# Kernel optimization log

Measured on AMD Instinct MI355X. Metric: run time of the kernel, lower is better.

## Reference

```python
import jax, jax.numpy as jnp
import numpy as np
import math

B, NH, DIM = 8, 12, 768
NP, NF = 196, 16            # n (patches per frame), num_frames
DH = DIM // NH              # 64
D3 = 3 * DH                 # per-head feature dim after projection (192)
SEQ = NP * NF               # 3136 body tokens (+1 cls)
ROT = DH                    # rotary dim (RotaryEmbedding(dim=64))
SCALE = 1.0 / (math.sqrt(DH) * NH)


def _heads(t):
    b, s, _ = t.shape
    return t.reshape(b, s, NH, D3).transpose(0, 2, 1, 3)  # b h s d


def _rope(x):
    # lucidrains-style interleaved rotary on the first ROT dims of each head
    s = x.shape[2]
    inv_freq = 1.0 / (10000.0 ** (jnp.arange(0, ROT, 2, dtype=jnp.float32) / ROT))
    freqs = jnp.arange(s, dtype=jnp.float32)[:, None] * inv_freq  # [s, ROT/2]
    freqs = jnp.repeat(freqs, 2, axis=-1)                          # [s, ROT]
    cos, sin = jnp.cos(freqs), jnp.sin(freqs)
    xr, xp = x[..., :ROT], x[..., ROT:]
    x1, x2 = xr[..., ::2], xr[..., 1::2]
    half = jnp.stack((-x2, x1), axis=-1).reshape(xr.shape)
    return jnp.concatenate([xr * cos + half * sin, xp], axis=-1)


def _att_sum(q, k, v):
    # softmax(q k^T * SCALE) v, then sum over queries keepdim (dim 2)
    p = jax.nn.softmax(jnp.einsum('bhqd,bhkd->bhqk', q, k) * SCALE, axis=-1)
    return jnp.einsum('bhqk,bhkd->bhqd', p, v).sum(axis=2, keepdims=True)


def setup_inputs():
    key = jax.random.key(0)
    ks = jax.random.split(key, 11)
    p = lambda k, sh: jax.random.normal(k, sh, jnp.float32) * 0.02
    return {
        'x': jax.random.normal(ks[0], (B, SEQ + 1, DIM), jnp.float32),
        'Wq': p(ks[1], (DIM, 3 * DIM)), 'bq': p(ks[2], (3 * DIM,)),
        'Wk': p(ks[3], (DIM, 3 * DIM)), 'bk': p(ks[4], (3 * DIM,)),
        'Wv': p(ks[5], (DIM, 3 * DIM)), 'bv': p(ks[6], (3 * DIM,)),
        'Wt': p(ks[7], (3 * DIM, DIM)), 'bt': p(ks[8], (DIM,)),
        'Wf': p(ks[9], (3 * DIM, DIM)), 'bf': p(ks[10], (DIM,)),
    }


def reference(x, Wq, bq, Wk, bk, Wv, bv, Wt, bt, Wf, bf):
    body = x[:, 1:, :]
    # NOTE: the original swaps k/v projections for body tokens (k_mat uses self.v, v_mat uses self.k)
    q = _rope(_heads(body @ Wq + bq))
    k = _rope(_heads(body @ Wv + bv))
    v = _heads(body @ Wk + bk)

    # cls-token attention over the full sequence (correct k/v mapping here)
    q_cls = _heads(x[:, 0:1, :] @ Wq + bq)          # [b,h,1,d]
    k_cls = _heads(x @ Wk + bk)
    v_cls = _heads(x @ Wv + bv)
    p_cls = jax.nn.softmax(jnp.einsum('bhqd,bhkd->bhqk', q_cls, k_cls) * SCALE, axis=-1)
    cls_out = jnp.einsum('bhqk,bhkd->bhqd', p_cls, v_cls)  # [b,h,1,d]

    # temporal attention per spatial position x = 1..NP-1, vectorized
    # token index t = f*NP + x  ->  reshape [b,h,NF,NP,d], move spatial first
    qg = q.reshape(B, NH, NF, NP, D3).transpose(0, 1, 3, 2, 4)[:, :, 1:]  # [b,h,NP-1,NF,d]
    kg = k.reshape(B, NH, NF, NP, D3).transpose(0, 1, 3, 2, 4)[:, :, 1:]
    vg = v.reshape(B, NH, NF, NP, D3).transpose(0, 1, 3, 2, 4)[:, :, 1:]
    pg = jax.nn.softmax(jnp.einsum('bhxfd,bhxgd->bhxfg', qg, kg) * SCALE, axis=-1)
    tmp = jnp.einsum('bhxfg,bhxgd->bhxfd', pg, vg).sum(axis=3)  # sum over query frames -> [b,h,NP-1,d]

    temporal = jnp.tile(tmp, (1, 1, NF, 1))  # torch .repeat tiles -> [b,h,(NP-1)*NF,d]
    ti = temporal.transpose(0, 2, 1, 3).reshape(B, (NP - 1) * NF, NH * D3) @ Wt + bt

    # second pass (q uses self.q, v uses self.k, k uses self.v per original)
    q2 = _heads(ti @ Wq + bq)
    v2 = _heads(ti @ Wk + bk)
    k2 = _heads(ti @ Wv + bv)
    outs = [_att_sum(q2[:, :, 0:NP], k2[:, :, 0:NP], v2[:, :, 0:NP])]
    for xi in range(1, NF):  # small fixed loop over frames
        outs.append(_att_sum(q2[:, :, xi:xi + NP], k2[:, :, xi::NP], v2[:, :, xi::NP]))
    t2 = jnp.concatenate(outs, axis=2)        # [b,h,NF,d]
    t2 = jnp.tile(t2, (1, 1, NP, 1))          # [b,h,SEQ,d]
    t2 = jnp.concatenate([cls_out, t2], axis=2)  # [b,h,SEQ+1,d]
    return t2.transpose(0, 2, 1, 3).reshape(B, SEQ + 1, NH * D3) @ Wf + bf
```

## Files before the change

kernel.cpp:

```cpp
#include <hip/hip_runtime.h>
#include <cstdint>
#include <cstddef>


typedef unsigned short u16;
typedef __attribute__((ext_vector_type(8))) short short8;
typedef __attribute__((ext_vector_type(4))) float f32x4;

#define DEV static __device__ __forceinline__
#define AS1 __attribute__((address_space(1)))
#define AS3 __attribute__((address_space(3)))

DEV float b2f(u16 u) { union { unsigned int i; float f; } v; v.i = ((unsigned int)u) << 16; return v.f; }
DEV float b2fs(short s) { return b2f((u16)s); }
DEV u16 f2b(float f) {
    union { float f; unsigned int i; } v; v.f = f;
    unsigned int r = v.i + 0x7fffu + ((v.i >> 16) & 1u);
    return (u16)(r >> 16);
}
DEV void gld16(const u16* g, u16* l) {
    __builtin_amdgcn_global_load_lds((AS1 void*)(g), (AS3 void*)(l), 16, 0, 0);
}

DEV int detect_fl(const u16* x) {
    int lane = threadIdx.x & 63;
    const u16* p = x + lane * 8;
    int c = 0;
#pragma unroll
    for (int j = 0; j < 8; j++) c += (((p[j] >> 7) & 0xFFu) >= 134u);
#pragma unroll
    for (int off = 32; off; off >>= 1) c += __shfl_xor(c, off);
    return c > 8;
}

constexpr int   ROWS  = 3137;
constexpr int   NPm1  = 195;
constexpr int   MT    = 8 * NPm1;
constexpr int   N3    = 2304;
constexpr float SCALE = 1.0f / 96.0f;
constexpr size_t P2Z  = (size_t)MT * N3;
constexpr int   CLS_NS = 32;
constexpr int   CLS_RS = 99;
constexpr int   LDK   = 200;

DEV float wave_max(float v) {
#pragma unroll
    for (int off = 32; off; off >>= 1) v = fmaxf(v, __shfl_xor(v, off));
    return v;
}
DEV float wave_sum(float v) {
#pragma unroll
    for (int off = 32; off; off >>= 1) v += __shfl_xor(v, off);
    return v;
}
DEV float block_max256(float v, float* red) {
    v = wave_max(v);
    __syncthreads();
    if ((threadIdx.x & 63) == 0) red[threadIdx.x >> 6] = v;
    __syncthreads();
    return fmaxf(fmaxf(red[0], red[1]), fmaxf(red[2], red[3]));
}
DEV float block_sum256(float v, float* red) {
    v = wave_sum(v);
    __syncthreads();
    if ((threadIdx.x & 63) == 0) red[threadIdx.x >> 6] = v;
    __syncthreads();
    return (red[0] + red[1]) + (red[2] + red[3]);
}

DEV void do_transpose(const void* in, u16* out, int R, int C,
                      int bx, int by, int fl, u16 (*tls)[33]) {
    int tx = threadIdx.x & 31, ty = threadIdx.x >> 5;
#pragma unroll
    for (int i = 0; i < 32; i += 8) {
        int r = by + ty + i, c = bx + tx;
        size_t idx = (size_t)r * C + c;
        tls[ty + i][tx] = fl ? f2b(((const float*)in)[idx]) : ((const u16*)in)[idx];
    }
    __syncthreads();
#pragma unroll
    for (int i = 0; i < 32; i += 8) {
        int c = bx + ty + i, r = by + tx;
        out[(size_t)c * R + r] = tls[tx][ty + i];
    }
}

__global__ __launch_bounds__(256) void prep(const u16* __restrict__ x,
                                            const void* __restrict__ Wq,
                                            const void* __restrict__ Wk,
                                            const void* __restrict__ Wv,
                                            const void* __restrict__ Wt,
                                            const void* __restrict__ Wf,
                                            u16* __restrict__ WT,
                                            u16* __restrict__ WtT,
                                            u16* __restrict__ WfT,
                                            u16* __restrict__ xb,
                                            float* __restrict__ wacc,
                                            float* __restrict__ ropeT,
                                            int usexb) {
    __shared__ u16 tls[32][33];
    int bid = blockIdx.x;
    if (bid < 5184) {
        int fl = detect_fl(x);
        int z = bid / 1728, t = bid % 1728;
        const void* W = (z == 0) ? Wq : (z == 1) ? Wk : Wv;
        do_transpose(W, WT + (size_t)z * N3 * 768, 768, N3,
                     (t % 72) * 32, (t / 72) * 32, fl, tls);
        return;
    }
    bid -= 5184;
    if (bid < 3456) {
        int fl = detect_fl(x);
        int z = bid / 1728, t = bid % 1728;
        do_transpose(z ? Wf : Wt, z ? WfT : WtT, N3, 768,
                     (t % 24) * 32, (t / 24) * 32, fl, tls);
        return;
    }
    bid -= 3456;
    if (bid < 9411) {
        if (!usexb) return;
        int fl = detect_fl(x);
        size_t e0 = ((size_t)bid * 256 + threadIdx.x) * 8;
        if (fl) {
            const float* p = (const float*)x + e0;
            float4 u0 = *(const float4*)p, u1 = *(const float4*)(p + 4);
            short8 r;
            r[0]=(short)f2b(u0.x); r[1]=(short)f2b(u0.y); r[2]=(short)f2b(u0.z); r[3]=(short)f2b(u0.w);
            r[4]=(short)f2b(u1.x); r[5]=(short)f2b(u1.y); r[6]=(short)f2b(u1.z); r[7]=(short)f2b(u1.w);
            *(short8*)(xb + e0) = r;
        } else {
            *(short8*)(xb + e0) = *(const short8*)(x + e0);
        }
        return;
    }
    bid -= 9411;
    if (bid < 1176) {
        wacc[(size_t)bid * 256 + threadIdx.x] = 0.f;
        return;
    }
    bid -= 1176;
    {
        int t = bid * 256 + threadIdx.x;
        int s = t >> 5, i = t & 31;
        float inv = powf(10000.0f, -(float)(2 * i) * (1.0f / 64.0f));
        float sn, cs;
        sincosf((float)s * inv, &sn, &cs);
        ropeT[t * 2]     = cs;
        ropeT[t * 2 + 1] = sn;
    }
}

DEV short8 pack_f32x8(const float* p) {
    const float4 u0 = *(const float4*)p;
    const float4 u1 = *(const float4*)(p + 4);
    short8 r;
    r[0]=(short)f2b(u0.x); r[1]=(short)f2b(u0.y); r[2]=(short)f2b(u0.z); r[3]=(short)f2b(u0.w);
    r[4]=(short)f2b(u1.x); r[5]=(short)f2b(u1.y); r[6]=(short)f2b(u1.z); r[7]=(short)f2b(u1.w);
    return r;
}

__global__ __launch_bounds__(256) void gemm_bt(const void* __restrict__ A, size_t aoff,
                                               const u16* __restrict__ BT,
                                               const void* __restrict__ b0p,
                                               const void* __restrict__ b1p,
                                               const void* __restrict__ b2p,
                                               void* __restrict__ C,
                                               int M, int N, int K,
                                               const u16* __restrict__ xdet,
                                               int araw, int cf32) {
    const int fl = detect_fl(xdet);
    const int af32 = araw && fl;
    const int z = blockIdx.z;
    const u16* Bz = BT + (size_t)z * N * K;
    const void* bias = (z == 0) ? b0p : (z == 1) ? b1p : b2p;

    __shared__ u16 As[128 * 32];
    __shared__ u16 Bs[128 * 32];

    const int tid  = threadIdx.x;
    const int lane = tid & 63;
    const int wave = tid >> 6;
    const int wm   = wave & 1;
    const int wn   = wave >> 1;
    const int quad = lane >> 4;
    const int l16  = lane & 15;

    const int m0 = blockIdx.y * 128;
    const int n0 = blockIdx.x * 128;

    f32x4 acc[4][4] = {};

    if (!af32) {
        const u16* Ab = (const u16*)A + aoff;
        int srow = wave * 32 + (lane >> 2);
        int scol = (lane & 3) * 8;
        int ar0 = m0 + srow;      if (ar0 > M - 1) ar0 = M - 1;
        int ar1 = m0 + srow + 16; if (ar1 > M - 1) ar1 = M - 1;
        const u16* gA0 = Ab + (size_t)ar0 * K + scol;
        const u16* gA1 = Ab + (size_t)ar1 * K + scol;
        const u16* gB0 = Bz + (size_t)(n0 + srow) * K + scol;
        const u16* gB1 = Bz + (size_t)(n0 + srow + 16) * K + scol;
        u16* lA0 = As + wave * 1024;
        u16* lA1 = As + wave * 1024 + 512;
        u16* lB0 = Bs + wave * 1024;
        u16* lB1 = Bs + wave * 1024 + 512;

        for (int k0 = 0; k0 < K; k0 += 32) {
            __syncthreads();
            gld16(gA0 + k0, lA0);
            gld16(gA1 + k0, lA1);
            gld16(gB0 + k0, lB0);
            gld16(gB1 + k0, lB1);
            __syncthreads();

            short8 af[4], bfr[4];
#pragma unroll
            for (int i = 0; i < 4; i++)
                af[i] = *(const short8*)(&As[(wm * 64 + i * 16 + l16) * 32 + quad * 8]);
#pragma unroll
            for (int j = 0; j < 4; j++)
                bfr[j] = *(const short8*)(&Bs[(wn * 64 + j * 16 + l16) * 32 + quad * 8]);
#pragma unroll
            for (int i = 0; i < 4; i++)
#pragma unroll
                for (int j = 0; j < 4; j++)
                    acc[i][j] = __builtin_amdgcn_mfma_f32_16x16x32_bf16(af[i], bfr[j], acc[i][j], 0, 0, 0);
        }
    } else {
        const int r0 = tid >> 2;
        const int kp = (tid & 3) << 3;
        int ga0 = m0 + r0;       if (ga0 > M - 1) ga0 = M - 1;
        int ga1 = m0 + r0 + 64;  if (ga1 > M - 1) ga1 = M - 1;
        const size_t arow0 = aoff + (size_t)ga0 * K + kp;
        const size_t arow1 = aoff + (size_t)ga1 * K + kp;
        const u16* Bp0 = Bz + (size_t)(n0 + r0) * K + kp;
        const u16* Bp1 = Bz + (size_t)(n0 + r0 + 64) * K + kp;

        for (int k0 = 0; k0 < K; k0 += 32) {
            short8 a0 = pack_f32x8((const float*)A + arow0 + k0);
            short8 a1 = pack_f32x8((const float*)A + arow1 + k0);
            short8 bv0 = *(const short8*)(Bp0 + k0);
            short8 bv1 = *(const short8*)(Bp1 + k0);
            __syncthreads();
            *(short8*)(&As[r0 * 32 + kp])        = a0;
            *(short8*)(&As[(r0 + 64) * 32 + kp]) = a1;
            *(short8*)(&Bs[r0 * 32 + kp])        = bv0;
            *(short8*)(&Bs[(r0 + 64) * 32 + kp]) = bv1;
            __syncthreads();

            short8 af[4], bfr[4];
#pragma unroll
            for (int i = 0; i < 4; i++)
                af[i] = *(const short8*)(&As[(wm * 64 + i * 16 + l16) * 32 + quad * 8]);
#pragma unroll
            for (int j = 0; j < 4; j++)
                bfr[j] = *(const short8*)(&Bs[(wn * 64 + j * 16 + l16) * 32 + quad * 8]);
#pragma unroll
            for (int i = 0; i < 4; i++)
#pragma unroll
                for (int j = 0; j < 4; j++)
                    acc[i][j] = __builtin_amdgcn_mfma_f32_16x16x32_bf16(af[i], bfr[j], acc[i][j], 0, 0, 0);
        }
    }

#pragma unroll
    for (int j = 0; j < 4; j++) {
        int col = n0 + wn * 64 + j * 16 + l16;
        float bb = fl ? ((const float*)bias)[col] : b2f(((const u16*)bias)[col]);
#pragma unroll
        for (int i = 0; i < 4; i++) {
            int rowb = m0 + wm * 64 + i * 16 + quad * 4;
#pragma unroll
            for (int r = 0; r < 4; r++) {
                int row = rowb + r;
                if (row < M) {
                    size_t idx = (size_t)z * M * N + (size_t)row * N + col;
                    float v = acc[i][j][r] + bb;
                    if (cf32) ((float*)C)[idx] = v;
                    else      ((u16*)C)[idx]  = f2b(v);
                }
            }
        }
    }
}

__global__ __launch_bounds__(256) void phaseA_attn(const u16* __restrict__ Pb, size_t PZv,
                                                   const float* __restrict__ tab,
                                                   u16* __restrict__ tmp,
                                                   float* __restrict__ clsP, int b0) {
    __shared__ __align__(16) char smem[40800];
    int xg = blockIdx.x, h = blockIdx.y, bl = blockIdx.z;
    int b = b0 + bl;
    int tid = threadIdx.x;

    if (xg < 195) {
        int p = xg + 1;
        u16* Qs = (u16*)smem;
        u16* Ks = Qs + 16 * LDK;
        u16* Vs = Ks + 16 * LDK;
        float* w = (float*)(smem + 3 * 16 * LDK * 2);
        const u16* Pq = Pb;
        const u16* Pk = Pb + 2 * PZv;
        const u16* Pv = Pb + PZv;
        const size_t rbase = (size_t)bl * ROWS;

        for (int i = tid; i < 384; i += 256) {
            int f = i / 24, c = (i % 24) * 8;
            int s = f * 196 + p;
            size_t gidx = (rbase + 1 + s) * N3 + (size_t)h * 192 + c;
            short8 q8 = *(const short8*)(Pq + gidx);
            short8 k8 = *(const short8*)(Pk + gidx);
            short8 v8 = *(const short8*)(Pv + gidx);
            if (c < 64) {
                const float* tp = tab + ((size_t)s * 32 + (c >> 1)) * 2;
                float4 t0 = *(const float4*)tp;
                float4 t1 = *(const float4*)(tp + 4);
                float cs[4] = {t0.x, t0.z, t1.x, t1.z};
                float sn[4] = {t0.y, t0.w, t1.y, t1.w};
                short8 qo, ko;
#pragma unroll
                for (int j = 0; j < 4; j++) {
                    float q1 = b2fs(q8[2 * j]), q2 = b2fs(q8[2 * j + 1]);
                    float k1 = b2fs(k8[2 * j]), k2 = b2fs(k8[2 * j + 1]);
                    qo[2 * j]     = (short)f2b(q1 * cs[j] - q2 * sn[j]);
                    qo[2 * j + 1] = (short)f2b(q2 * cs[j] + q1 * sn[j]);
                    ko[2 * j]     = (short)f2b(k1 * cs[j] - k2 * sn[j]);
                    ko[2 * j + 1] = (short)f2b(k2 * cs[j] + k1 * sn[j]);
                }
                q8 = qo; k8 = ko;
            }
            *(short8*)&Qs[f * LDK + c] = q8;
            *(short8*)&Ks[f * LDK + c] = k8;
            *(short8*)&Vs[f * LDK + c] = v8;
        }
        __syncthreads();

        if (tid < 64) {
            int quad = tid >> 4, l16 = tid & 15;
            short8 Af[6], Bf[6];
#pragma unroll
            for (int ks = 0; ks < 6; ks++) {
                Af[ks] = *(const short8*)&Qs[l16 * LDK + quad * 8 + ks * 32];
                Bf[ks] = *(const short8*)&Ks[l16 * LDK + quad * 8 + ks * 32];
            }
            f32x4 S = {0.f, 0.f, 0.f, 0.f};
#pragma unroll
            for (int ks = 0; ks < 6; ks++)
                S = __builtin_amdgcn_mfma_f32_16x16x32_bf16(Af[ks], Bf[ks], S, 0, 0, 0);
            float wcol = 0.f;
#pragma unroll
            for (int r = 0; r < 4; r++) {
                float v = S[r] * SCALE;
                float m = v;
#pragma unroll
                for (int k = 1; k < 16; k <<= 1) m = fmaxf(m, __shfl_xor(m, k));
                float e = __expf(v - m);
                float l = e;
#pragma unroll
                for (int k = 1; k < 16; k <<= 1) l += __shfl_xor(l, k);
                wcol += e / l;
            }
            wcol += __shfl_xor(wcol, 16);
            wcol += __shfl_xor(wcol, 32);
            if (quad == 0) w[l16] = wcol;
        }
        __syncthreads();

        if (tid < 192) {
            float acc = 0.f;
#pragma unroll
            for (int g = 0; g < 16; g++) acc += w[g] * b2f(Vs[g * LDK + tid]);
            tmp[(size_t)(b * NPm1 + p - 1) * N3 + (size_t)h * 192 + tid] = f2b(acc);
        }
    } else {
        int sp = xg - 195;
        int base = sp * CLS_RS;
        int cnt = ROWS - base; if (cnt > CLS_RS) cnt = CLS_RS;
        u16* Ksh  = (u16*)smem;
        float* qs  = (float*)(smem + CLS_RS * LDK * 2);
        float* sc  = qs + 192;
        float* red = sc + 100;
        const size_t hbase = (size_t)bl * ROWS * N3 + (size_t)h * 192;
        const u16* Pq  = Pb;
        const u16* Pkc = Pb + PZv;
        const u16* Pvc = Pb + 2 * PZv;

        if (tid < 192) qs[tid] = b2f(Pq[hbase + tid]);
        for (int i = tid; i < cnt * 24; i += 256) {
            int r = i / 24, c = (i % 24) * 8;
            *(short8*)&Ksh[r * LDK + c] =
                *(const short8*)(Pkc + hbase + (size_t)(base + r) * N3 + c);
        }
        __syncthreads();

        float sval = -1e30f;
        if (tid < cnt) {
            float s = 0.f;
#pragma unroll
            for (int c = 0; c < 24; c++) {
                short8 v8 = *(const short8*)&Ksh[tid * LDK + c * 8];
#pragma unroll
                for (int j = 0; j < 8; j++) s += qs[c * 8 + j] * b2fs(v8[j]);
            }
            sval = s * SCALE;
        }
        float m = block_max256(sval, red);
        float e = (tid < cnt) ? __expf(sval - m) : 0.f;
        float l = block_sum256(e, red);
        if (tid < cnt) sc[tid] = e;
        __syncthreads();

        float* pp = clsP + ((size_t)(b * 12 + h) * CLS_NS + sp) * 194;
        if (tid == 0) { pp[0] = m; pp[1] = l; }
        if (tid < 192) {
            float acc = 0.f;
            const u16* vb = Pvc + hbase + tid;
            for (int r = 0; r < cnt; r++) acc += sc[r] * b2f(vb[(size_t)(base + r) * N3]);
            pp[2 + tid] = acc;
        }
    }
}

__global__ __launch_bounds__(256) void attn2_sc(const u16* __restrict__ P2,
                                                float* __restrict__ wacc) {
    int t = blockIdx.x, h = blockIdx.y, b = blockIdx.z;
    __shared__ u16 Ks[195 * LDK];
    __shared__ u16 Qs[31 * LDK];
    __shared__ float pm[4][16], ps[4][16];
    int tid = threadIdx.x;
    const size_t hb = (size_t)b * NPm1 * N3 + (size_t)h * 192;
    const u16* Q  = P2;
    const u16* Kc = P2 + 2 * P2Z;

    for (int i = tid; i < 195 * 24; i += 256) {
        int r = i / 24, c = (i % 24) * 8;
        *(short8*)&Ks[r * LDK + c] = *(const short8*)(Kc + hb + (size_t)r * N3 + c);
    }
    for (int i = tid; i < 31 * 24; i += 256) {
        int r = i / 24, c = (i % 24) * 8;
        int qr = (t * 16 + r) % 195;
        *(short8*)&Qs[r * LDK + c] = *(const short8*)(Q + hb + (size_t)qr * N3 + c);
    }
    __syncthreads();

    int wave = tid >> 6, lane = tid & 63, quad = lane >> 4, l16 = lane & 15;
    float* wb = wacc + (size_t)((b * 12 + h) * 16) * 196;

    for (int xi = 1 + wave; xi <= 15; xi += 4) {
        short8 Af[6], Bf[6];
#pragma unroll
        for (int ks = 0; ks < 6; ks++) {
            Af[ks] = *(const short8*)&Qs[(xi + l16) * LDK + quad * 8 + ks * 32];
            Bf[ks] = *(const short8*)&Ks[(xi + l16) * LDK + quad * 8 + ks * 32];
        }
        f32x4 S = {0.f, 0.f, 0.f, 0.f};
#pragma unroll
        for (int ks = 0; ks < 6; ks++)
            S = __builtin_amdgcn_mfma_f32_16x16x32_bf16(Af[ks], Bf[ks], S, 0, 0, 0);
        float wcol = 0.f;
#pragma unroll
        for (int r = 0; r < 4; r++) {
            float v = S[r] * SCALE;
            float m = v;
#pragma unroll
            for (int k = 1; k < 16; k <<= 1) m = fmaxf(m, __shfl_xor(m, k));
            float e = __expf(v - m);
            float l = e;
#pragma unroll
            for (int k = 1; k < 16; k <<= 1) l += __shfl_xor(l, k);
            bool qok = (t * 16 + quad * 4 + r) <= 195;
            wcol += qok ? e / l : 0.f;
        }
        wcol += __shfl_xor(wcol, 16);
        wcol += __shfl_xor(wcol, 32);
        if (quad == 0) atomicAdd(&wb[xi * 196 + l16], wcol);
    }

    short8 Af0[6];
#pragma unroll
    for (int ks = 0; ks < 6; ks++)
        Af0[ks] = *(const short8*)&Qs[l16 * LDK + quad * 8 + ks * 32];

    f32x4 Sc[4];
    int   cl[4];
    int   cn = 0;
    for (int c = wave; c < 13; c += 4) {
        int g = c * 16 + l16;
        int krow = g % 195;
        short8 Bf[6];
#pragma unroll
        for (int ks = 0; ks < 6; ks++)
            Bf[ks] = *(const short8*)&Ks[krow * LDK + quad * 8 + ks * 32];
        f32x4 S = {0.f, 0.f, 0.f, 0.f};
#pragma unroll
        for (int ks = 0; ks < 6; ks++)
            S = __builtin_amdgcn_mfma_f32_16x16x32_bf16(Af0[ks], Bf[ks], S, 0, 0, 0);
        bool kbad = g > 195;
#pragma unroll
        for (int r = 0; r < 4; r++) S[r] = kbad ? -1e30f : S[r] * SCALE;
        Sc[cn] = S; cl[cn] = c; cn++;
    }
#pragma unroll
    for (int r = 0; r < 4; r++) {
        float v = -1e30f;
        for (int n = 0; n < cn; n++) v = fmaxf(v, Sc[n][r]);
#pragma unroll
        for (int k = 1; k < 16; k <<= 1) v = fmaxf(v, __shfl_xor(v, k));
        if (l16 == 0) pm[wave][quad * 4 + r] = v;
    }
    __syncthreads();
    float gmx[4], tot[4];
#pragma unroll
    for (int r = 0; r < 4; r++) {
        int qr = quad * 4 + r;
        gmx[r] = fmaxf(fmaxf(pm[0][qr], pm[1][qr]), fmaxf(pm[2][qr], pm[3][qr]));
    }
#pragma unroll
    for (int r = 0; r < 4; r++) {
        float s = 0.f;
        for (int n = 0; n < cn; n++) {
            float e = __expf(Sc[n][r] - gmx[r]);
            Sc[n][r] = e;
            s += e;
        }
#pragma unroll
        for (int k = 1; k < 16; k <<= 1) s += __shfl_xor(s, k);
        if (l16 == 0) ps[wave][quad * 4 + r] = s;
    }
    __syncthreads();
#pragma unroll
    for (int r = 0; r < 4; r++) {
        int qr = quad * 4 + r;
        tot[r] = (ps[0][qr] + ps[1][qr]) + (ps[2][qr] + ps[3][qr]);
    }
    for (int n = 0; n < cn; n++) {
        float wv = 0.f;
#pragma unroll
        for (int r = 0; r < 4; r++) {
            bool qok = (t * 16 + quad * 4 + r) <= 195;
            wv += qok ? Sc[n][r] / tot[r] : 0.f;
        }
        wv += __shfl_xor(wv, 16);
        wv += __shfl_xor(wv, 32);
        int g = cl[n] * 16 + l16;
        if (quad == 0 && g <= 195) atomicAdd(&wb[g], wv);
    }
}

__global__ __launch_bounds__(192) void fin(const u16* __restrict__ P2,
                                           const float* __restrict__ wacc,
                                           const float* __restrict__ clsP,
                                           u16* __restrict__ Fmat) {
    int xg = blockIdx.x, h = blockIdx.y, b = blockIdx.z;
    int tid = threadIdx.x;
    if (xg == 0) {
        const float* p0 = clsP + (size_t)(b * 12 + h) * CLS_NS * 194;
        float M = -1e30f;
#pragma unroll
        for (int s = 0; s < CLS_NS; s++) M = fmaxf(M, p0[s * 194]);
        float L = 0.f, acc = 0.f;
#pragma unroll
        for (int s = 0; s < CLS_NS; s++) {
            float w = __expf(p0[s * 194] - M);
            L += w * p0[s * 194 + 1];
            acc += w * p0[s * 194 + 2 + tid];
        }
        Fmat[(size_t)(b * 17) * N3 + (size_t)h * 192 + tid] = f2b(acc / L);
    } else {
        int xi = xg - 1;
        int Nk = (xi == 0) ? 196 : 16;
        const u16* V = P2 + P2Z;
        const size_t hb = (size_t)b * NPm1 * N3 + (size_t)h * 192;
        const float* wb = wacc + (size_t)((b * 12 + h) * 16 + xi) * 196;
        float acc = 0.f;
        for (int g = 0; g < Nk; g++) {
            int kr = (xi == 0) ? (g % 195) : (xi + g);
            acc += wb[g] * b2f(V[hb + (size_t)kr * N3 + tid]);
        }
        Fmat[(size_t)(b * 17 + 1 + xi) * N3 + (size_t)h * 192 + tid] = f2b(acc);
    }
}

__global__ __launch_bounds__(256) void scatter_out(const float* __restrict__ F17,
                                                   void* __restrict__ out,
                                                   const u16* __restrict__ xdet) {
    const int fl = detect_fl(xdet);
    int t = blockIdx.x * 256 + threadIdx.x;
    int c = t % 96;
    int rem = t / 96;
    int s = rem % ROWS;
    int b = rem / ROWS;
    int src = b * 17 + (s == 0 ? 0 : 1 + ((s - 1) & 15));
    const float* sp = F17 + ((size_t)src * 96 + c) * 8;
    if (fl) {
        float* o = (float*)out + (size_t)t * 8;
        *(float4*)o       = *(const float4*)sp;
        *(float4*)(o + 4) = *(const float4*)(sp + 4);
    } else {
        u16* o = (u16*)out + (size_t)t * 8;
        short8 v;
#pragma unroll
        for (int j = 0; j < 8; j++) v[j] = (short)f2b(sp[j]);
        *(short8*)o = v;
    }
}

extern "C" void kernel_launch(void* const* d_in, const int* in_sizes, int n_in,
                              void* d_out, int out_size, void* d_ws, size_t ws_size,
                              hipStream_t stream) {
    const void* x   = d_in[0];
    const void* Wq  = d_in[1];
    const void* bq  = d_in[2];
    const void* Wk  = d_in[3];
    const void* bk  = d_in[4];
    const void* Wv  = d_in[5];
    const void* bv  = d_in[6];
    const void* Wt  = d_in[7];
    const void* bt  = d_in[8];
    const void* Wf  = d_in[9];
    const void* bfb = d_in[10];
    const u16* xdet = (const u16*)x;
    (void)in_sizes; (void)n_in; (void)out_size;

    auto al = [](size_t b) { return (b + 255) & ~(size_t)255; };
    const size_t szWT   = al((size_t)3 * N3 * 768 * 2);
    const size_t szWtT  = al((size_t)768 * N3 * 2);
    const size_t szTmp  = al((size_t)MT * N3 * 2);
    const size_t szFmat = al((size_t)136 * N3 * 2);
    const size_t szRope = al((size_t)3136 * 32 * 2 * 4);
    const size_t szClsP = al((size_t)8 * 12 * CLS_NS * 194 * 4);
    const size_t szWacc = al((size_t)96 * 16 * 196 * 4);
    const size_t szXb   = al((size_t)8 * ROWS * 768 * 2);
    const size_t szB    = al(3 * P2Z * 2) + al((size_t)MT * 768 * 2) +
                          al((size_t)136 * 768 * 4);
    const size_t basePerst = szWT + 2 * szWtT + szTmp + szFmat + szRope + szClsP + szWacc;

    int bs = 1; int usexb = 0;
    {
        const int cand[4] = {8, 4, 2, 1};
        for (int i = 0; i < 4; i++) {
            size_t szP = al((size_t)3 * cand[i] * ROWS * N3 * 2);
            size_t need = basePerst + szXb + (szP > szB ? szP : szB);
            if (ws_size >= need) { bs = cand[i]; usexb = 1; break; }
        }
        if (!usexb) {
            size_t szP = al((size_t)3 * ROWS * N3 * 2);
            size_t need = basePerst + (szP > szB ? szP : szB);
            if (ws_size < need) return;
        }
    }

    char* ws = (char*)d_ws;
    size_t off = 0;
    auto allocB = [&](size_t bytes) { char* p = ws + off; off += al(bytes); return p; };
    u16*   WT    = (u16*)allocB((size_t)3 * N3 * 768 * 2);
    u16*   WtT   = (u16*)allocB((size_t)768 * N3 * 2);
    u16*   WfT   = (u16*)allocB((size_t)768 * N3 * 2);
    u16*   tmp   = (u16*)allocB((size_t)MT * N3 * 2);
    u16*   Fmat  = (u16*)allocB((size_t)136 * N3 * 2);
    float* ropeT = (float*)allocB((size_t)3136 * 32 * 2 * 4);
    float* clsP  = (float*)allocB((size_t)8 * 12 * CLS_NS * 194 * 4);
    float* wacc  = (float*)allocB((size_t)96 * 16 * 196 * 4);
    u16*   xb    = usexb ? (u16*)allocB((size_t)8 * ROWS * 768 * 2) : nullptr;
    size_t aliasOff = off;
    u16* Pb = (u16*)allocB((size_t)3 * bs * ROWS * N3 * 2);
    off = aliasOff;
    u16*   P2  = (u16*)allocB(3 * P2Z * 2);
    u16*   tiu = (u16*)allocB((size_t)MT * 768 * 2);
    float* F17 = (float*)allocB((size_t)136 * 768 * 4);

    const size_t PZv = (size_t)bs * ROWS * N3;

    prep<<<dim3(19619), 256, 0, stream>>>(xdet, Wq, Wk, Wv, Wt, Wf,
                                          WT, WtT, WfT, xb, wacc, ropeT, usexb);

    for (int b0 = 0; b0 < 8; b0 += bs) {
        int Mv = bs * ROWS;
        size_t aoff = (size_t)b0 * ROWS * 768;
        if (usexb)
            gemm_bt<<<dim3(18, (Mv + 127) / 128, 3), 256, 0, stream>>>(
                xb, aoff, WT, bq, bk, bv, Pb, Mv, N3, 768, xdet, 0, 0);
        else
            gemm_bt<<<dim3(18, (Mv + 127) / 128, 3), 256, 0, stream>>>(
                x, aoff, WT, bq, bk, bv, Pb, Mv, N3, 768, xdet, 1, 0);
        phaseA_attn<<<dim3(227, 12, bs), 256, 0, stream>>>(Pb, PZv, ropeT, tmp, clsP, b0);
    }

    gemm_bt<<<dim3(6, 13, 1), 256, 0, stream>>>(tmp, 0, WtT, bt, bt, bt, tiu,
                                                MT, 768, N3, xdet, 0, 0);
    gemm_bt<<<dim3(18, 13, 3), 256, 0, stream>>>(tiu, 0, WT, bq, bk, bv, P2,
                                                 MT, N3, 768, xdet, 0, 0);
    attn2_sc<<<dim3(13, 12, 8), 256, 0, stream>>>(P2, wacc);
    fin<<<dim3(17, 12, 8), 192, 0, stream>>>(P2, wacc, clsP, Fmat);
    gemm_bt<<<dim3(6, 2, 1), 256, 0, stream>>>(Fmat, 0, WfT, bfb, bfb, bfb, F17,
                                               136, 768, N3, xdet, 0, 1);
    scatter_out<<<dim3(9411), 256, 0, stream>>>(F17, d_out, xdet);
}
```

Baseline: 1.163 ms.

## Add 256x256 double-buffered MFMA GEMM for the QKV projection

Adds a new 512-thread GEMM kernel with 256x256 tiles, double-buffered LDS filled by global_load_lds, an XOR swizzle, interleaved LDS reads and MFMA phases with priority hints, and an XCD-aware block remap. It replaces the 128x128 gemm_bt for the large body QKV projection when the bf16 copy of x is available. Biases are pre-converted to fp32 in the prep kernel, so the epilogue no longer needs a per-element dtype branch. The larger tiles aim to raise arithmetic intensity and overlap loads with compute, but they use 128KB of LDS, which limits occupancy to one block per CU, and they waste work on the padded last M tile.

```diff
diff --git a/kernel.cpp b/kernel.cpp
--- a/kernel.cpp
+++ b/kernel.cpp
@@ -60,7 +60,7 @@
     __syncthreads();
     return fmaxf(fmaxf(red[0], red[1]), fmaxf(red[2], red[3]));
 }
-DEV float block_sum256(float v, float* red) {
+float __device__ __forceinline__ block_sum256(float v, float* red) {
     v = wave_sum(v);
     __syncthreads();
     if ((threadIdx.x & 63) == 0) red[threadIdx.x >> 6] = v;
@@ -91,12 +91,16 @@
                                             const void* __restrict__ Wv,
                                             const void* __restrict__ Wt,
                                             const void* __restrict__ Wf,
+                                            const void* __restrict__ bq,
+                                            const void* __restrict__ bk,
+                                            const void* __restrict__ bv,
                                             u16* __restrict__ WT,
                                             u16* __restrict__ WtT,
                                             u16* __restrict__ WfT,
                                             u16* __restrict__ xb,
                                             float* __restrict__ wacc,
                                             float* __restrict__ ropeT,
+                                            float* __restrict__ biasF,
                                             int usexb) {
     __shared__ u16 tls[32][33];
     int bid = blockIdx.x;
@@ -139,7 +143,7 @@
         return;
     }
     bid -= 1176;
-    {
+    if (bid < 392) {
         int t = bid * 256 + threadIdx.x;
         int s = t >> 5, i = t & 31;
         float inv = powf(10000.0f, -(float)(2 * i) * (1.0f / 64.0f));
@@ -147,6 +151,15 @@
         sincosf((float)s * inv, &sn, &cs);
         ropeT[t * 2]     = cs;
         ropeT[t * 2 + 1] = sn;
+        return;
+    }
+    bid -= 392;
+    {
+        int fl = detect_fl(x);
+        int t = bid * 256 + threadIdx.x;
+        int z = t / 2304, i = t - z * 2304;
+        const void* b = (z == 0) ? bq : (z == 1) ? bk : bv;
+        biasF[t] = fl ? ((const float*)b)[i] : b2f(((const u16*)b)[i]);
     }
 }
 
@@ -279,6 +292,140 @@
                     if (cf32) ((float*)C)[idx] = v;
                     else      ((u16*)C)[idx]  = f2b(v);
                 }
+            }
+        }
+    }
+}
+
+__global__ __launch_bounds__(512) void gemm256(const u16* __restrict__ A, size_t aoff,
+                                               const u16* __restrict__ BT,
+                                               const float* __restrict__ biasF,
+                                               u16* __restrict__ C,
+                                               int M, int N, int K) {
+    __shared__ __align__(16) u16 As[2][16384];
+    __shared__ __align__(16) u16 Bs[2][16384];
+
+    const int tid  = threadIdx.x;
+    const int lane = tid & 63;
+    const int wid  = tid >> 6;
+    const int wm   = wid >> 2;
+    const int wn   = wid & 3;
+    const int quad = lane >> 4;
+    const int l16  = lane & 15;
+    const int z    = blockIdx.z;
+
+    const int NTN  = N >> 8;
+    const int nwg  = gridDim.x;
+    const int orig = blockIdx.x;
+    const int q8 = nwg >> 3, r8 = nwg & 7, xcd = orig & 7;
+    const int wg = (xcd < r8 ? xcd * (q8 + 1) : r8 * (q8 + 1) + (xcd - r8) * q8)
+                   + (orig >> 3);
+    const int n0 = (wg % NTN) * 256;
+    const int m0 = (wg / NTN) * 256;
+
+    const u16* Ab = A + aoff;
+    const u16* Bz = BT + (size_t)z * N * K;
+    const int  Mc = M - 1;
+
+    const int srow = (wid << 3) + ((lane >> 3));
+    const int sc   = (lane & 7) << 3;
+    const u16* gA[4]; const u16* gB[4];
+#pragma unroll
+    for (int h = 0; h < 2; h++)
+#pragma unroll
+        for (int l = 0; l < 2; l++) {
+            int rl = h * 128 + l * 64 + srow;
+            int cs = sc ^ ((rl & 4) ? 16 : 0);
+            int gr = m0 + rl; if (gr > Mc) gr = Mc;
+            gA[h * 2 + l] = Ab + (size_t)gr * K + cs;
+            gB[h * 2 + l] = Bz + (size_t)(n0 + rl) * K + cs;
+        }
+
+    f32x4  acc[8][4] = {};
+    short8 aF[4][2], bF[2][2];
+
+    const int csw   = (quad << 3) ^ ((l16 & 4) ? 16 : 0);
+    const int aBase = (wm * 128 + l16) * 64 + csw;
+    const int bBase = (wn * 64  + l16) * 64 + csw;
+
+#define STG_A(b, h, kt) do { _Pragma("unroll")                                 \
+    for (int _l = 0; _l < 2; _l++)                                             \
+        gld16(gA[(h) * 2 + _l] + ((kt) << 6),                                  \
+              &As[b][(((h) * 128 + _l * 64 + (wid << 3)) << 6)]); } while (0)
+#define STG_B(b, h, kt) do { _Pragma("unroll")                                 \
+    for (int _l = 0; _l < 2; _l++)                                             \
+        gld16(gB[(h) * 2 + _l] + ((kt) << 6),                                  \
+              &Bs[b][(((h) * 128 + _l * 64 + (wid << 3)) << 6)]); } while (0)
+#define RD_A(b, mh) do { _Pragma("unroll")                                     \
+    for (int _m = 0; _m < 4; _m++) {                                           \
+        aF[_m][0] = *(const short8*)&As[b][aBase + (mh) * 4096 + _m * 1024];   \
+        aF[_m][1] = *(const short8*)&As[b][aBase + (mh) * 4096 + _m * 1024 + 32]; } } while (0)
+#define RD_B(b, nh) do { _Pragma("unroll")                                     \
+    for (int _n = 0; _n < 2; _n++) {                                           \
+        bF[_n][0] = *(const short8*)&Bs[b][bBase + (nh) * 2048 + _n * 1024];   \
+        bF[_n][1] = *(const short8*)&Bs[b][bBase + (nh) * 2048 + _n * 1024 + 32]; } } while (0)
+#define MM(mh, nh) do {                                                        \
+    __builtin_amdgcn_s_setprio(1);                                             \
+    _Pragma("unroll") for (int _ks = 0; _ks < 2; _ks++)                        \
+    _Pragma("unroll") for (int _m = 0; _m < 4; _m++)                           \
+    _Pragma("unroll") for (int _n = 0; _n < 2; _n++)                           \
+        acc[(mh) * 4 + _m][(nh) * 2 + _n] =                                    \
+            __builtin_amdgcn_mfma_f32_16x16x32_bf16(aF[_m][_ks], bF[_n][_ks],  \
+                acc[(mh) * 4 + _m][(nh) * 2 + _n], 0, 0, 0);                   \
+    __builtin_amdgcn_s_setprio(0); } while (0)
+#define BARR  __builtin_amdgcn_s_barrier()
+#define LGKM0 asm volatile("s_waitcnt lgkmcnt(0)" ::: "memory")
+#define VMC(n) asm volatile("s_waitcnt vmcnt(" #n ")" ::: "memory")
+
+    STG_A(0, 0, 0); STG_A(0, 1, 0); STG_B(0, 0, 0); STG_B(0, 1, 0);
+    STG_A(1, 0, 1);
+    VMC(2); BARR;
+
+    const int NP2 = K >> 7;
+    for (int i = 0; i < NP2 - 1; i++) {
+        const int kt1 = 2 * i + 1, kt2 = 2 * i + 2, kt3 = 2 * i + 3;
+        RD_A(0, 0); RD_B(0, 0); STG_A(1, 1, kt1); BARR; LGKM0; MM(0, 0);         BARR;
+        RD_B(0, 1);             STG_B(1, 0, kt1); BARR; LGKM0; MM(0, 1);         BARR;
+        RD_A(0, 1);             STG_B(1, 1, kt1); BARR; LGKM0; MM(1, 1);         BARR;
+        RD_B(0, 0);             STG_A(0, 0, kt2); BARR; LGKM0; MM(1, 0); VMC(2); BARR;
+        RD_A(1, 0); RD_B(1, 0); STG_A(0, 1, kt2); BARR; LGKM0; MM(0, 0);         BARR;
+        RD_B(1, 1);             STG_B(0, 0, kt2); BARR; LGKM0; MM(0, 1);         BARR;
+        RD_A(1, 1);             STG_B(0, 1, kt2); BARR; LGKM0; MM(1, 1);         BARR;
+        RD_B(1, 0);             STG_A(1, 0, kt3); BARR; LGKM0; MM(1, 0); VMC(2); BARR;
+    }
+    {
+        const int ktb = 2 * NP2 - 1;
+        RD_A(0, 0); RD_B(0, 0); STG_A(1, 1, ktb); BARR; LGKM0; MM(0, 0);         BARR;
+        RD_B(0, 1);             STG_B(1, 0, ktb); BARR; LGKM0; MM(0, 1);         BARR;
+        RD_A(0, 1);             STG_B(1, 1, ktb); BARR; LGKM0; MM(1, 1);         BARR;
+        RD_B(0, 0);                               BARR; LGKM0; MM(1, 0); VMC(0); BARR;
+        RD_A(1, 0); RD_B(1, 0);                   BARR; LGKM0; MM(0, 0);         BARR;
+        RD_B(1, 1);                               BARR; LGKM0; MM(0, 1);         BARR;
+        RD_A(1, 1);                               BARR; LGKM0; MM(1, 1);         BARR;
+        RD_B(1, 0);                               BARR; LGKM0; MM(1, 0);
+    }
+#undef STG_A
+#undef STG_B
+#undef RD_A
+#undef RD_B
+#undef MM
+#undef BARR
+#undef LGKM0
+#undef VMC
+
+#pragma unroll
+    for (int ni = 0; ni < 4; ni++) {
+        int gcol = n0 + wn * 64 + ni * 16 + l16;
+        float bb = biasF[z * N + gcol];
+#pragma unroll
+        for (int mi = 0; mi < 8; mi++) {
+            int rowb = m0 + wm * 128 + mi * 16 + quad * 4;
+#pragma unroll
+            for (int r = 0; r < 4; r++) {
+                int row = rowb + r;
+                if (row < M)
+                    C[(size_t)z * M * N + (size_t)row * N + gcol] =
+                        f2b(acc[mi][ni][r] + bb);
             }
         }
     }
@@ -630,10 +777,12 @@
     const size_t szRope = al((size_t)3136 * 32 * 2 * 4);
     const size_t szClsP = al((size_t)8 * 12 * CLS_NS * 194 * 4);
     const size_t szWacc = al((size_t)96 * 16 * 196 * 4);
+    const size_t szBias = al((size_t)3 * N3 * 4);
     const size_t szXb   = al((size_t)8 * ROWS * 768 * 2);
     const size_t szB    = al(3 * P2Z * 2) + al((size_t)MT * 768 * 2) +
                           al((size_t)136 * 768 * 4);
-    const size_t basePerst = szWT + 2 * szWtT + szTmp + szFmat + szRope + szClsP + szWacc;
+    const size_t basePerst = szWT + 2 * szWtT + szTmp + szFmat + szRope +
+                             szClsP + szWacc + szBias;
 
     int bs = 1; int usexb = 0;
     {
@@ -661,6 +810,7 @@
     float* ropeT = (float*)allocB((size_t)3136 * 32 * 2 * 4);
     float* clsP  = (float*)allocB((size_t)8 * 12 * CLS_NS * 194 * 4);
     float* wacc  = (float*)allocB((size_t)96 * 16 * 196 * 4);
+    float* biasF = (float*)allocB((size_t)3 * N3 * 4);
     u16*   xb    = usexb ? (u16*)allocB((size_t)8 * ROWS * 768 * 2) : nullptr;
     size_t aliasOff = off;
     u16* Pb = (u16*)allocB((size_t)3 * bs * ROWS * N3 * 2);
@@ -671,18 +821,21 @@
 
     const size_t PZv = (size_t)bs * ROWS * N3;
 
-    prep<<<dim3(19619), 256, 0, stream>>>(xdet, Wq, Wk, Wv, Wt, Wf,
-                                          WT, WtT, WfT, xb, wacc, ropeT, usexb);
+    prep<<<dim3(19646), 256, 0, stream>>>(xdet, Wq, Wk, Wv, Wt, Wf, bq, bk, bv,
+                                          WT, WtT, WfT, xb, wacc, ropeT, biasF,
+                                          usexb);
 
     for (int b0 = 0; b0 < 8; b0 += bs) {
         int Mv = bs * ROWS;
         size_t aoff = (size_t)b0 * ROWS * 768;
-        if (usexb)
-            gemm_bt<<<dim3(18, (Mv + 127) / 128, 3), 256, 0, stream>>>(
-                xb, aoff, WT, bq, bk, bv, Pb, Mv, N3, 768, xdet, 0, 0);
-        else
+        if (usexb) {
+            int mtiles = (Mv + 255) >> 8;
+            gemm256<<<dim3(9 * mtiles, 1, 3), 512, 0, stream>>>(
+                xb, aoff, WT, biasF, Pb, Mv, N3, 768);
+        } else {
             gemm_bt<<<dim3(18, (Mv + 127) / 128, 3), 256, 0, stream>>>(
                 x, aoff, WT, bq, bk, bv, Pb, Mv, N3, 768, xdet, 1, 0);
+        }
         phaseA_attn<<<dim3(227, 12, bs), 256, 0, stream>>>(Pb, PZv, ropeT, tmp, clsP, b0);
     }
 
```

New measurement: 1.175 ms. No clear change (+1.0%).
